# Kernel tuning notes

Measured on AMD Instinct MI355X. Metric: run time of the kernel, lower is better.

The kernel has to match this reference:

```python
import jax, jax.numpy as jnp
import numpy as np

T, B, C = 2048, 4, 1024
H, K = 16, 15
PAD_L = 14  # causal: padding_l = K - 1


def setup_inputs() -> dict:
    key = jax.random.key(0)
    k1, k2 = jax.random.split(key)
    x = jax.random.normal(k1, (T, B, C), dtype=jnp.float32)
    # xavier_uniform for Linear(C, H*K): bound = sqrt(6/(fan_in+fan_out))
    bound = float(np.sqrt(6.0 / (C + H * K)))
    Wlin = jax.random.uniform(k2, (H * K, C), dtype=jnp.float32, minval=-bound, maxval=bound)
    return {"x": x, "Wlin": Wlin}


def reference(x, Wlin):
    # x: (T, B, C); Wlin: (H*K, C) -- weight_linear with no bias
    t, b, c = x.shape
    r = c // H  # channels per head
    # Generate per-position filters: (T, B, H, K)
    w = jnp.einsum('tbc,kc->tbk', x, Wlin).reshape(t, b, H, K)
    # weight_softmax=True: normalize over kernel taps
    w = jax.nn.softmax(w, axis=-1)
    # unfold1d: pad left PAD_L, right K-1-PAD_L along time, take K shifted views
    xp = jnp.pad(x, ((PAD_L, K - 1 - PAD_L), (0, 0), (0, 0)))
    # (T, B, C, K): tap k at output t reads padded position t+k
    xu = jnp.stack([xp[k:k + t] for k in range(K)], axis=-1)
    xu = xu.reshape(t, b, H, r, K)
    # batched tiny matmul: (R x K) @ (K x 1) per (t, b, h)
    out = jnp.einsum('tbhrk,tbhk->tbhr', xu, w)
    return out.reshape(t, b, c)
```

## Files before the change

kernel.cpp:

```cpp
#include <hip/hip_runtime.h>
#include <hip/hip_bf16.h>


#define T_DIM 2048
#define B_DIM 4
#define C_DIM 1024
#define H_DIM 16
#define K_TAPS 15
#define R_DIM 64
#define N_DIM (H_DIM * K_TAPS)
#define M_DIM (T_DIM * B_DIM)
#define SM_STRIDE 244

typedef __attribute__((ext_vector_type(8))) short bf16x8;
typedef __attribute__((ext_vector_type(4))) float f32x4;

__device__ __forceinline__ unsigned short f2bf(float f) {
    union { float f; unsigned u; } v; v.f = f;
    return (unsigned short)((v.u + 0x7FFFu + ((v.u >> 16) & 1u)) >> 16);
}

__global__ __launch_bounds__(256) void convert_w(
    const float* __restrict__ W, unsigned short* __restrict__ Wbf)
{
    int i = (blockIdx.x * 256 + threadIdx.x) * 4;
    float4 v = *reinterpret_cast<const float4*>(W + i);
    ushort4 o;
    o.x = f2bf(v.x); o.y = f2bf(v.y); o.z = f2bf(v.z); o.w = f2bf(v.w);
    *reinterpret_cast<ushort4*>(Wbf + i) = o;
}

__global__ __launch_bounds__(256) void gemm_softmax_mfma(
    const float* __restrict__ x, const unsigned short* __restrict__ Wbf,
    float* __restrict__ wbuf)
{
    __shared__ float sm[4][16][SM_STRIDE];

    const int tid = threadIdx.x;
    const int w   = tid >> 6;
    const int l   = tid & 63;
    const int m0  = blockIdx.x * 16;
    const int row = l & 15;
    const int kg  = l >> 4;

    f32x4 acc[15];
    #pragma unroll
    for (int nt = 0; nt < 15; ++nt) acc[nt] = (f32x4){0.f, 0.f, 0.f, 0.f};

    const float* xp = x + (size_t)(m0 + row) * C_DIM + w * 256 + kg * 8;
    const unsigned short* wp = Wbf + (size_t)row * C_DIM + w * 256 + kg * 8;

    #pragma unroll 2
    for (int ks = 0; ks < 8; ++ks) {
        const int k = ks * 32;
        float4 a0 = *reinterpret_cast<const float4*>(xp + k);
        float4 a1 = *reinterpret_cast<const float4*>(xp + k + 4);
        bf16x8 af;
        af[0] = (short)f2bf(a0.x); af[1] = (short)f2bf(a0.y);
        af[2] = (short)f2bf(a0.z); af[3] = (short)f2bf(a0.w);
        af[4] = (short)f2bf(a1.x); af[5] = (short)f2bf(a1.y);
        af[6] = (short)f2bf(a1.z); af[7] = (short)f2bf(a1.w);
        bf16x8 bfr[15];
        #pragma unroll
        for (int nt = 0; nt < 15; ++nt)
            bfr[nt] = *reinterpret_cast<const bf16x8*>(wp + (size_t)nt * 16 * C_DIM + k);
        #pragma unroll
        for (int nt = 0; nt < 15; ++nt)
            acc[nt] = __builtin_amdgcn_mfma_f32_16x16x32_bf16(af, bfr[nt], acc[nt], 0, 0, 0);
    }

    #pragma unroll
    for (int nt = 0; nt < 15; ++nt)
        #pragma unroll
        for (int j = 0; j < 4; ++j)
            sm[w][kg * 4 + j][nt * 16 + row] = acc[nt][j];
    __syncthreads();

    const int r = tid >> 4;
    const int h = tid & 15;
    float s[K_TAPS];
    #pragma unroll
    for (int kk = 0; kk < K_TAPS; ++kk) {
        const int c = h * K_TAPS + kk;
        s[kk] = sm[0][r][c] + sm[1][r][c] + sm[2][r][c] + sm[3][r][c];
    }
    float mx = s[0];
    #pragma unroll
    for (int kk = 1; kk < K_TAPS; ++kk) mx = fmaxf(mx, s[kk]);
    float sum = 0.f;
    #pragma unroll
    for (int kk = 0; kk < K_TAPS; ++kk) {
        s[kk] = __expf(s[kk] - mx);
        sum += s[kk];
    }
    const float inv = 1.f / sum;
    float* dst = wbuf + (size_t)(m0 + r) * N_DIM + h * K_TAPS;
    #pragma unroll
    for (int kk = 0; kk < K_TAPS; ++kk) dst[kk] = s[kk] * inv;
}

__global__ __launch_bounds__(256) void conv_kernel(
    const float* __restrict__ x, const float* __restrict__ wbuf,
    float* __restrict__ out)
{
    __shared__ float xs[64 + K_TAPS - 1][R_DIM];

    const int tid = threadIdx.x;
    const int t0 = blockIdx.x * 64;
    const int bh = blockIdx.y;
    const int b = bh >> 4;
    const int h = bh & 15;
    const int cbase = h * R_DIM;

    for (int idx = tid; idx < (64 + K_TAPS - 1) * 16; idx += 256) {
        int rrow = idx >> 4, q = idx & 15;
        int t = t0 - (K_TAPS - 1) + rrow;
        float4 v = (t >= 0)
            ? *reinterpret_cast<const float4*>(x + ((size_t)t * B_DIM + b) * C_DIM + cbase + q * 4)
            : (float4){0.f, 0.f, 0.f, 0.f};
        *reinterpret_cast<float4*>(&xs[rrow][q * 4]) = v;
    }
    __syncthreads();

    const int r = tid & 63;
    const int tg = __builtin_amdgcn_readfirstlane(tid >> 6);

    float xv[31];
    #pragma unroll
    for (int j = 0; j < 31; ++j) xv[j] = xs[tg * 16 + j][r];

    float accv[16];
    #pragma unroll
    for (int i = 0; i < 16; ++i) accv[i] = 0.f;

    #pragma unroll
    for (int i = 0; i < 16; ++i) {
        const int t = t0 + tg * 16 + i;
        const float* wv = wbuf + ((size_t)t * B_DIM + b) * N_DIM + h * K_TAPS;
        #pragma unroll
        for (int k = 0; k < K_TAPS; ++k)
            accv[i] += wv[k] * xv[i + k];
    }

    #pragma unroll
    for (int i = 0; i < 16; ++i) {
        const int t = t0 + tg * 16 + i;
        out[((size_t)t * B_DIM + b) * C_DIM + cbase + r] = accv[i];
    }
}

extern "C" void kernel_launch(void* const* d_in, const int* in_sizes, int n_in,
                              void* d_out, int out_size, void* d_ws, size_t ws_size,
                              hipStream_t stream) {
    const float* x    = (const float*)d_in[0];
    const float* Wlin = (const float*)d_in[1];
    float* out  = (float*)d_out;

    float* wbuf = (float*)d_ws;
    unsigned short* Wbf = (unsigned short*)((char*)d_ws + (size_t)M_DIM * N_DIM * sizeof(float));

    convert_w<<<(N_DIM * C_DIM) / (256 * 4), 256, 0, stream>>>(Wlin, Wbf);
    gemm_softmax_mfma<<<M_DIM / 16, 256, 0, stream>>>(x, Wbf, wbuf);
    conv_kernel<<<dim3(T_DIM / 64, B_DIM * H_DIM), 256, 0, stream>>>(x, wbuf, out);
}
```

Baseline: 127.9 us.

## Fuse filter GEMM, softmax and dynamic convolution into one MFMA kernel

Merges the softmax-filter GEMM and the convolution kernel into one kernel per (16-timestep, batch) tile. The normalized filters are written as a banded bf16 Toeplitz matrix in shared memory, and the convolution runs as MFMA against a transposed bf16 copy of the x window. The intermediate weight buffer round trip through global memory and one launch go away, and x loads are hoisted ahead of the GEMM loop. In exchange the conv inputs and filters are rounded to bf16, which lowers accuracy, and each tile re-reads a 14-step halo of x.

```diff
diff --git a/kernel.cpp b/kernel.cpp
--- a/kernel.cpp
+++ b/kernel.cpp
@@ -7,10 +7,11 @@
 #define C_DIM 1024
 #define H_DIM 16
 #define K_TAPS 15
-#define R_DIM 64
-#define N_DIM (H_DIM * K_TAPS)
-#define M_DIM (T_DIM * B_DIM)
+#define N_DIM 240
 #define SM_STRIDE 244
+#define SM_FLOATS (4 * 16 * SM_STRIDE)
+#define XT_STRIDE 34
+#define XT_OFF 4096
 
 typedef __attribute__((ext_vector_type(8))) short bf16x8;
 typedef __attribute__((ext_vector_type(4))) float f32x4;
@@ -30,40 +31,45 @@
     *reinterpret_cast<ushort4*>(Wbf + i) = o;
 }
 
-__global__ __launch_bounds__(256) void gemm_softmax_mfma(
+__global__ __launch_bounds__(256, 2) void fused_dynconv(
     const float* __restrict__ x, const unsigned short* __restrict__ Wbf,
-    float* __restrict__ wbuf)
+    float* __restrict__ out)
 {
-    __shared__ float sm[4][16][SM_STRIDE];
+    __shared__ float smem[SM_FLOATS];
 
     const int tid = threadIdx.x;
-    const int w   = tid >> 6;
+    const int wv  = tid >> 6;
     const int l   = tid & 63;
-    const int m0  = blockIdx.x * 16;
+    const int t0  = blockIdx.x * 16;
+    const int b   = blockIdx.y;
     const int row = l & 15;
     const int kg  = l >> 4;
+
+    const float* xp = x + ((size_t)(t0 + row) * B_DIM + b) * C_DIM + wv * 256 + kg * 8;
+    const unsigned short* wp = Wbf + (size_t)row * C_DIM + wv * 256 + kg * 8;
+
+    float4 xa[8], xb[8];
+    #pragma unroll
+    for (int ks = 0; ks < 8; ++ks) {
+        xa[ks] = *reinterpret_cast<const float4*>(xp + ks * 32);
+        xb[ks] = *reinterpret_cast<const float4*>(xp + ks * 32 + 4);
+    }
 
     f32x4 acc[15];
     #pragma unroll
     for (int nt = 0; nt < 15; ++nt) acc[nt] = (f32x4){0.f, 0.f, 0.f, 0.f};
 
-    const float* xp = x + (size_t)(m0 + row) * C_DIM + w * 256 + kg * 8;
-    const unsigned short* wp = Wbf + (size_t)row * C_DIM + w * 256 + kg * 8;
-
-    #pragma unroll 2
+    #pragma unroll
     for (int ks = 0; ks < 8; ++ks) {
-        const int k = ks * 32;
-        float4 a0 = *reinterpret_cast<const float4*>(xp + k);
-        float4 a1 = *reinterpret_cast<const float4*>(xp + k + 4);
-        bf16x8 af;
-        af[0] = (short)f2bf(a0.x); af[1] = (short)f2bf(a0.y);
-        af[2] = (short)f2bf(a0.z); af[3] = (short)f2bf(a0.w);
-        af[4] = (short)f2bf(a1.x); af[5] = (short)f2bf(a1.y);
-        af[6] = (short)f2bf(a1.z); af[7] = (short)f2bf(a1.w);
         bf16x8 bfr[15];
         #pragma unroll
         for (int nt = 0; nt < 15; ++nt)
-            bfr[nt] = *reinterpret_cast<const bf16x8*>(wp + (size_t)nt * 16 * C_DIM + k);
+            bfr[nt] = *reinterpret_cast<const bf16x8*>(wp + (size_t)nt * 16 * C_DIM + ks * 32);
+        bf16x8 af;
+        af[0] = (short)f2bf(xa[ks].x); af[1] = (short)f2bf(xa[ks].y);
+        af[2] = (short)f2bf(xa[ks].z); af[3] = (short)f2bf(xa[ks].w);
+        af[4] = (short)f2bf(xb[ks].x); af[5] = (short)f2bf(xb[ks].y);
+        af[6] = (short)f2bf(xb[ks].z); af[7] = (short)f2bf(xb[ks].w);
         #pragma unroll
         for (int nt = 0; nt < 15; ++nt)
             acc[nt] = __builtin_amdgcn_mfma_f32_16x16x32_bf16(af, bfr[nt], acc[nt], 0, 0, 0);
@@ -73,79 +79,80 @@
     for (int nt = 0; nt < 15; ++nt)
         #pragma unroll
         for (int j = 0; j < 4; ++j)
-            sm[w][kg * 4 + j][nt * 16 + row] = acc[nt][j];
+            smem[(wv * 16 + kg * 4 + j) * SM_STRIDE + nt * 16 + row] = acc[nt][j];
     __syncthreads();
 
-    const int r = tid >> 4;
-    const int h = tid & 15;
-    float s[K_TAPS];
+    const int rr = tid >> 4;
+    const int hh = tid & 15;
+    float wn[K_TAPS];
     #pragma unroll
     for (int kk = 0; kk < K_TAPS; ++kk) {
-        const int c = h * K_TAPS + kk;
-        s[kk] = sm[0][r][c] + sm[1][r][c] + sm[2][r][c] + sm[3][r][c];
+        const int c = hh * K_TAPS + kk;
+        wn[kk] = smem[(0 * 16 + rr) * SM_STRIDE + c] + smem[(1 * 16 + rr) * SM_STRIDE + c]
+               + smem[(2 * 16 + rr) * SM_STRIDE + c] + smem[(3 * 16 + rr) * SM_STRIDE + c];
     }
-    float mx = s[0];
+    float mx = wn[0];
     #pragma unroll
-    for (int kk = 1; kk < K_TAPS; ++kk) mx = fmaxf(mx, s[kk]);
+    for (int kk = 1; kk < K_TAPS; ++kk) mx = fmaxf(mx, wn[kk]);
     float sum = 0.f;
     #pragma unroll
-    for (int kk = 0; kk < K_TAPS; ++kk) {
-        s[kk] = __expf(s[kk] - mx);
-        sum += s[kk];
-    }
+    for (int kk = 0; kk < K_TAPS; ++kk) { wn[kk] = __expf(wn[kk] - mx); sum += wn[kk]; }
     const float inv = 1.f / sum;
-    float* dst = wbuf + (size_t)(m0 + r) * N_DIM + h * K_TAPS;
-    #pragma unroll
-    for (int kk = 0; kk < K_TAPS; ++kk) dst[kk] = s[kk] * inv;
-}
+    __syncthreads();
 
-__global__ __launch_bounds__(256) void conv_kernel(
-    const float* __restrict__ x, const float* __restrict__ wbuf,
-    float* __restrict__ out)
-{
-    __shared__ float xs[64 + K_TAPS - 1][R_DIM];
-
-    const int tid = threadIdx.x;
-    const int t0 = blockIdx.x * 64;
-    const int bh = blockIdx.y;
-    const int b = bh >> 4;
-    const int h = bh & 15;
-    const int cbase = h * R_DIM;
-
-    for (int idx = tid; idx < (64 + K_TAPS - 1) * 16; idx += 256) {
-        int rrow = idx >> 4, q = idx & 15;
-        int t = t0 - (K_TAPS - 1) + rrow;
-        float4 v = (t >= 0)
-            ? *reinterpret_cast<const float4*>(x + ((size_t)t * B_DIM + b) * C_DIM + cbase + q * 4)
-            : (float4){0.f, 0.f, 0.f, 0.f};
-        *reinterpret_cast<float4*>(&xs[rrow][q * 4]) = v;
+    unsigned short* wsA = reinterpret_cast<unsigned short*>(smem);
+    {
+        int4 z = {0, 0, 0, 0};
+        int4* p = reinterpret_cast<int4*>(smem) + tid * 4;
+        p[0] = z; p[1] = z; p[2] = z; p[3] = z;
     }
     __syncthreads();
 
-    const int r = tid & 63;
-    const int tg = __builtin_amdgcn_readfirstlane(tid >> 6);
-
-    float xv[31];
     #pragma unroll
-    for (int j = 0; j < 31; ++j) xv[j] = xs[tg * 16 + j][r];
-
-    float accv[16];
-    #pragma unroll
-    for (int i = 0; i < 16; ++i) accv[i] = 0.f;
-
-    #pragma unroll
-    for (int i = 0; i < 16; ++i) {
-        const int t = t0 + tg * 16 + i;
-        const float* wv = wbuf + ((size_t)t * B_DIM + b) * N_DIM + h * K_TAPS;
-        #pragma unroll
-        for (int k = 0; k < K_TAPS; ++k)
-            accv[i] += wv[k] * xv[i + k];
+    for (int tap = 0; tap < K_TAPS; ++tap) {
+        const int k = rr + tap;
+        wsA[hh * 512 + (k >> 3) * 128 + rr * 8 + (k & 7)] = f2bf(wn[tap] * inv);
     }
 
-    #pragma unroll
-    for (int i = 0; i < 16; ++i) {
-        const int t = t0 + tg * 16 + i;
-        out[((size_t)t * B_DIM + b) * C_DIM + cbase + r] = accv[i];
+    unsigned short* xT = reinterpret_cast<unsigned short*>(smem + XT_OFF);
+    const int c4 = (tid & 127) * 4;
+    const int k2 = tid >> 7;
+    #pragma unroll 1
+    for (int q = 0; q < 2; ++q) {
+        #pragma unroll 4
+        for (int k = 0; k < 32; k += 2) {
+            const int kk = k + k2;
+            const int ta = t0 - 14 + kk;
+            float4 v = (ta >= 0 && ta < T_DIM)
+                ? *reinterpret_cast<const float4*>(x + ((size_t)ta * B_DIM + b) * C_DIM + q * 512 + c4)
+                : (float4){0.f, 0.f, 0.f, 0.f};
+            xT[(c4 + 0) * XT_STRIDE + kk] = f2bf(v.x);
+            xT[(c4 + 1) * XT_STRIDE + kk] = f2bf(v.y);
+            xT[(c4 + 2) * XT_STRIDE + kk] = f2bf(v.z);
+            xT[(c4 + 3) * XT_STRIDE + kk] = f2bf(v.w);
+        }
+        __syncthreads();
+
+        const int h0 = q * 8 + wv * 2;
+        const bf16x8 A0 = *reinterpret_cast<const bf16x8*>(wsA + (h0 * 64 + l) * 8);
+        const bf16x8 A1 = *reinterpret_cast<const bf16x8*>(wsA + ((h0 + 1) * 64 + l) * 8);
+        const int* xTi = reinterpret_cast<const int*>(xT);
+        #pragma unroll
+        for (int i = 0; i < 8; ++i) {
+            const int ct = q * 32 + wv * 8 + i;
+            const int cl = (wv * 8 + i) * 16 + row;
+            const int base = cl * (XT_STRIDE / 2) + kg * 4;
+            int4 bi;
+            bi.x = xTi[base + 0]; bi.y = xTi[base + 1];
+            bi.z = xTi[base + 2]; bi.w = xTi[base + 3];
+            union { int4 i4; bf16x8 h; } u; u.i4 = bi;
+            f32x4 d = __builtin_amdgcn_mfma_f32_16x16x32_bf16(
+                (i < 4) ? A0 : A1, u.h, (f32x4){0.f, 0.f, 0.f, 0.f}, 0, 0, 0);
+            #pragma unroll
+            for (int j = 0; j < 4; ++j)
+                out[((size_t)(t0 + kg * 4 + j) * B_DIM + b) * C_DIM + ct * 16 + row] = d[j];
+        }
+        __syncthreads();
     }
 }
 
@@ -154,12 +161,9 @@
                               hipStream_t stream) {
     const float* x    = (const float*)d_in[0];
     const float* Wlin = (const float*)d_in[1];
-    float* out  = (float*)d_out;
-
-    float* wbuf = (float*)d_ws;
-    unsigned short* Wbf = (unsigned short*)((char*)d_ws + (size_t)M_DIM * N_DIM * sizeof(float));
+    float* out = (float*)d_out;
+    unsigned short* Wbf = (unsigned short*)d_ws;
 
     convert_w<<<(N_DIM * C_DIM) / (256 * 4), 256, 0, stream>>>(Wlin, Wbf);
-    gemm_softmax_mfma<<<M_DIM / 16, 256, 0, stream>>>(x, Wbf, wbuf);
-    conv_kernel<<<dim3(T_DIM / 64, B_DIM * H_DIM), 256, 0, stream>>>(x, wbuf, out);
+    fused_dynconv<<<dim3(T_DIM / 16, B_DIM), 256, 0, stream>>>(x, Wbf, out);
 }
```

Result: faster. 125.1 us (-2.1%).

## Split filter GEMM over two N-halves and store softmax weights as bf16

Applied to the files above, without the earlier changes.

The projection GEMM is split across two blocks along the output dimension. Each block computes 8 of the 15 16-wide column tiles, with one overlapping tile, and runs softmax for 8 heads. This halves the accumulator registers, permits 4 blocks per CU, and doubles the grid. The softmax filter weights are now written to the workspace as bf16 instead of fp32, which halves the intermediate buffer traffic read by the conv kernel. The cost is that x is read twice in the GEMM and the filter weights lose precision.

```diff
diff --git a/kernel.cpp b/kernel.cpp
--- a/kernel.cpp
+++ b/kernel.cpp
@@ -8,9 +8,9 @@
 #define H_DIM 16
 #define K_TAPS 15
 #define R_DIM 64
-#define N_DIM (H_DIM * K_TAPS)
+#define N_DIM 240
 #define M_DIM (T_DIM * B_DIM)
-#define SM_STRIDE 244
+#define SM_STRIDE 132
 
 typedef __attribute__((ext_vector_type(8))) short bf16x8;
 typedef __attribute__((ext_vector_type(4))) float f32x4;
@@ -18,6 +18,10 @@
 __device__ __forceinline__ unsigned short f2bf(float f) {
     union { float f; unsigned u; } v; v.f = f;
     return (unsigned short)((v.u + 0x7FFFu + ((v.u >> 16) & 1u)) >> 16);
+}
+__device__ __forceinline__ float bf2f(unsigned short h) {
+    union { unsigned u; float f; } v; v.u = ((unsigned)h) << 16;
+    return v.f;
 }
 
 __global__ __launch_bounds__(256) void convert_w(
@@ -30,77 +34,79 @@
     *reinterpret_cast<ushort4*>(Wbf + i) = o;
 }
 
-__global__ __launch_bounds__(256) void gemm_softmax_mfma(
+__global__ __launch_bounds__(256, 4) void gemm_softmax_half(
     const float* __restrict__ x, const unsigned short* __restrict__ Wbf,
-    float* __restrict__ wbuf)
+    unsigned short* __restrict__ wout)
 {
     __shared__ float sm[4][16][SM_STRIDE];
 
     const int tid = threadIdx.x;
-    const int w   = tid >> 6;
+    const int wv  = tid >> 6;
     const int l   = tid & 63;
     const int m0  = blockIdx.x * 16;
+    const int nh  = blockIdx.y;
+    const int ntb = nh * 7;
     const int row = l & 15;
     const int kg  = l >> 4;
 
-    f32x4 acc[15];
+    f32x4 acc[8];
     #pragma unroll
-    for (int nt = 0; nt < 15; ++nt) acc[nt] = (f32x4){0.f, 0.f, 0.f, 0.f};
+    for (int nt = 0; nt < 8; ++nt) acc[nt] = (f32x4){0.f, 0.f, 0.f, 0.f};
 
-    const float* xp = x + (size_t)(m0 + row) * C_DIM + w * 256 + kg * 8;
-    const unsigned short* wp = Wbf + (size_t)row * C_DIM + w * 256 + kg * 8;
+    const float* xp = x + (size_t)(m0 + row) * C_DIM + wv * 256 + kg * 8;
+    const unsigned short* wp = Wbf + (size_t)(ntb * 16 + row) * C_DIM + wv * 256 + kg * 8;
 
     #pragma unroll 2
     for (int ks = 0; ks < 8; ++ks) {
         const int k = ks * 32;
         float4 a0 = *reinterpret_cast<const float4*>(xp + k);
         float4 a1 = *reinterpret_cast<const float4*>(xp + k + 4);
+        bf16x8 bfr[8];
+        #pragma unroll
+        for (int nt = 0; nt < 8; ++nt)
+            bfr[nt] = *reinterpret_cast<const bf16x8*>(wp + (size_t)nt * 16 * C_DIM + k);
         bf16x8 af;
         af[0] = (short)f2bf(a0.x); af[1] = (short)f2bf(a0.y);
         af[2] = (short)f2bf(a0.z); af[3] = (short)f2bf(a0.w);
         af[4] = (short)f2bf(a1.x); af[5] = (short)f2bf(a1.y);
         af[6] = (short)f2bf(a1.z); af[7] = (short)f2bf(a1.w);
-        bf16x8 bfr[15];
         #pragma unroll
-        for (int nt = 0; nt < 15; ++nt)
-            bfr[nt] = *reinterpret_cast<const bf16x8*>(wp + (size_t)nt * 16 * C_DIM + k);
-        #pragma unroll
-        for (int nt = 0; nt < 15; ++nt)
+        for (int nt = 0; nt < 8; ++nt)
             acc[nt] = __builtin_amdgcn_mfma_f32_16x16x32_bf16(af, bfr[nt], acc[nt], 0, 0, 0);
     }
 
     #pragma unroll
-    for (int nt = 0; nt < 15; ++nt)
+    for (int nt = 0; nt < 8; ++nt)
         #pragma unroll
         for (int j = 0; j < 4; ++j)
-            sm[w][kg * 4 + j][nt * 16 + row] = acc[nt][j];
+            sm[wv][kg * 4 + j][nt * 16 + row] = acc[nt][j];
     __syncthreads();
 
-    const int r = tid >> 4;
-    const int h = tid & 15;
-    float s[K_TAPS];
-    #pragma unroll
-    for (int kk = 0; kk < K_TAPS; ++kk) {
-        const int c = h * K_TAPS + kk;
-        s[kk] = sm[0][r][c] + sm[1][r][c] + sm[2][r][c] + sm[3][r][c];
+    if (tid < 128) {
+        const int rr = tid >> 3;
+        const int hh = tid & 7;
+        const int base = (nh ? 8 : 0) + hh * K_TAPS;
+        float s[K_TAPS];
+        #pragma unroll
+        for (int kk = 0; kk < K_TAPS; ++kk) {
+            const int c = base + kk;
+            s[kk] = sm[0][rr][c] + sm[1][rr][c] + sm[2][rr][c] + sm[3][rr][c];
+        }
+        float mx = s[0];
+        #pragma unroll
+        for (int kk = 1; kk < K_TAPS; ++kk) mx = fmaxf(mx, s[kk]);
+        float sum = 0.f;
+        #pragma unroll
+        for (int kk = 0; kk < K_TAPS; ++kk) { s[kk] = __expf(s[kk] - mx); sum += s[kk]; }
+        const float inv = 1.f / sum;
+        unsigned short* dst = wout + (size_t)(m0 + rr) * N_DIM + (nh * 8 + hh) * K_TAPS;
+        #pragma unroll
+        for (int kk = 0; kk < K_TAPS; ++kk) dst[kk] = f2bf(s[kk] * inv);
     }
-    float mx = s[0];
-    #pragma unroll
-    for (int kk = 1; kk < K_TAPS; ++kk) mx = fmaxf(mx, s[kk]);
-    float sum = 0.f;
-    #pragma unroll
-    for (int kk = 0; kk < K_TAPS; ++kk) {
-        s[kk] = __expf(s[kk] - mx);
-        sum += s[kk];
-    }
-    const float inv = 1.f / sum;
-    float* dst = wbuf + (size_t)(m0 + r) * N_DIM + h * K_TAPS;
-    #pragma unroll
-    for (int kk = 0; kk < K_TAPS; ++kk) dst[kk] = s[kk] * inv;
 }
 
 __global__ __launch_bounds__(256) void conv_kernel(
-    const float* __restrict__ x, const float* __restrict__ wbuf,
+    const float* __restrict__ x, const unsigned short* __restrict__ wbuf,
     float* __restrict__ out)
 {
     __shared__ float xs[64 + K_TAPS - 1][R_DIM];
@@ -136,10 +142,10 @@
     #pragma unroll
     for (int i = 0; i < 16; ++i) {
         const int t = t0 + tg * 16 + i;
-        const float* wv = wbuf + ((size_t)t * B_DIM + b) * N_DIM + h * K_TAPS;
+        const unsigned short* wv = wbuf + ((size_t)t * B_DIM + b) * N_DIM + h * K_TAPS;
         #pragma unroll
         for (int k = 0; k < K_TAPS; ++k)
-            accv[i] += wv[k] * xv[i + k];
+            accv[i] += bf2f(wv[k]) * xv[i + k];
     }
 
     #pragma unroll
@@ -154,12 +160,12 @@
                               hipStream_t stream) {
     const float* x    = (const float*)d_in[0];
     const float* Wlin = (const float*)d_in[1];
-    float* out  = (float*)d_out;
+    float* out = (float*)d_out;
 
-    float* wbuf = (float*)d_ws;
-    unsigned short* Wbf = (unsigned short*)((char*)d_ws + (size_t)M_DIM * N_DIM * sizeof(float));
+    unsigned short* wout = (unsigned short*)d_ws;
+    unsigned short* Wbf  = (unsigned short*)((char*)d_ws + (size_t)M_DIM * N_DIM * sizeof(unsigned short));
 
     convert_w<<<(N_DIM * C_DIM) / (256 * 4), 256, 0, stream>>>(Wlin, Wbf);
-    gemm_softmax_mfma<<<M_DIM / 16, 256, 0, stream>>>(x, Wbf, wbuf);
-    conv_kernel<<<dim3(T_DIM / 64, B_DIM * H_DIM), 256, 0, stream>>>(x, wbuf, out);
+    gemm_softmax_half<<<dim3(M_DIM / 16, 2), 256, 0, stream>>>(x, Wbf, wout);
+    conv_kernel<<<dim3(T_DIM / 64, B_DIM * H_DIM), 256, 0, stream>>>(x, wout, out);
 }
```

After: 148.0 us. +15.7%, slower.

## Pipeline GEMM x tiles through LDS with async global_load_lds triple buffering

Applied to the files above, without the earlier changes.

The projection GEMM is restructured. Each block now covers 32 rows with two waves, and each wave walks the full K dimension, so the cross-wave split-K reduction goes away. x tiles are staged into XOR-swizzled LDS through global_load_lds with a three-buffer prefetch pipeline. The softmax output is written padded to 16 taps per head with float4 stores, and the conv kernel indexes that padded layout. Each wave issues more weight-fragment loads per block, blocks are half the size, and the LDS footprint grows, which may hurt occupancy.

```diff
diff --git a/kernel.cpp b/kernel.cpp
--- a/kernel.cpp
+++ b/kernel.cpp
@@ -8,9 +8,13 @@
 #define H_DIM 16
 #define K_TAPS 15
 #define R_DIM 64
-#define N_DIM (H_DIM * K_TAPS)
-#define M_DIM (T_DIM * B_DIM)
-#define SM_STRIDE 244
+#define N_DIM 240
+#define M_DIM 8192
+#define BM 32
+#define BKF 128
+#define NSTEP 8
+#define TILE_F (BM * BKF)
+#define EP_STRIDE 244
 
 typedef __attribute__((ext_vector_type(8))) short bf16x8;
 typedef __attribute__((ext_vector_type(4))) float f32x4;
@@ -18,6 +22,12 @@
 __device__ __forceinline__ unsigned short f2bf(float f) {
     union { float f; unsigned u; } v; v.f = f;
     return (unsigned short)((v.u + 0x7FFFu + ((v.u >> 16) & 1u)) >> 16);
+}
+
+typedef __attribute__((address_space(1))) const void g_void;
+typedef __attribute__((address_space(3))) void l_void;
+__device__ __forceinline__ void gload_lds16(const void* g, void* l) {
+    __builtin_amdgcn_global_load_lds((g_void*)g, (l_void*)l, 16, 0, 0);
 }
 
 __global__ __launch_bounds__(256) void convert_w(
@@ -30,73 +40,107 @@
     *reinterpret_cast<ushort4*>(Wbf + i) = o;
 }
 
-__global__ __launch_bounds__(256) void gemm_softmax_mfma(
+__device__ __forceinline__ void stage_tile(const float* xrow0, int s, float* buf, int tid) {
+    #pragma unroll
+    for (int j = 0; j < 8; ++j) {
+        const int e  = j * 128 + tid;
+        const int r  = e >> 5;
+        const int c  = e & 31;
+        const int gc = c ^ (r & 7);
+        const float* src = xrow0 + (size_t)r * C_DIM + s * BKF + gc * 4;
+        float* dst = buf + (size_t)(j * 128 + (tid & ~63)) * 4;
+        gload_lds16(src, dst);
+    }
+}
+
+__global__ __launch_bounds__(128) void gemm_softmax_v3(
     const float* __restrict__ x, const unsigned short* __restrict__ Wbf,
-    float* __restrict__ wbuf)
+    float* __restrict__ wout)
 {
-    __shared__ float sm[4][16][SM_STRIDE];
+    __shared__ float smem[3 * TILE_F];
 
     const int tid = threadIdx.x;
-    const int w   = tid >> 6;
+    const int wv  = tid >> 6;
     const int l   = tid & 63;
-    const int m0  = blockIdx.x * 16;
+    const int m0  = blockIdx.x * BM;
     const int row = l & 15;
     const int kg  = l >> 4;
+    const int r7  = row & 7;
+
+    const float* xrow0 = x + (size_t)m0 * C_DIM;
+    const unsigned short* wp = Wbf + (size_t)row * C_DIM + kg * 8;
 
     f32x4 acc[15];
     #pragma unroll
     for (int nt = 0; nt < 15; ++nt) acc[nt] = (f32x4){0.f, 0.f, 0.f, 0.f};
 
-    const float* xp = x + (size_t)(m0 + row) * C_DIM + w * 256 + kg * 8;
-    const unsigned short* wp = Wbf + (size_t)row * C_DIM + w * 256 + kg * 8;
-
-    #pragma unroll 2
-    for (int ks = 0; ks < 8; ++ks) {
-        const int k = ks * 32;
-        float4 a0 = *reinterpret_cast<const float4*>(xp + k);
-        float4 a1 = *reinterpret_cast<const float4*>(xp + k + 4);
-        bf16x8 af;
-        af[0] = (short)f2bf(a0.x); af[1] = (short)f2bf(a0.y);
-        af[2] = (short)f2bf(a0.z); af[3] = (short)f2bf(a0.w);
-        af[4] = (short)f2bf(a1.x); af[5] = (short)f2bf(a1.y);
-        af[6] = (short)f2bf(a1.z); af[7] = (short)f2bf(a1.w);
-        bf16x8 bfr[15];
-        #pragma unroll
-        for (int nt = 0; nt < 15; ++nt)
-            bfr[nt] = *reinterpret_cast<const bf16x8*>(wp + (size_t)nt * 16 * C_DIM + k);
-        #pragma unroll
-        for (int nt = 0; nt < 15; ++nt)
-            acc[nt] = __builtin_amdgcn_mfma_f32_16x16x32_bf16(af, bfr[nt], acc[nt], 0, 0, 0);
-    }
-
+    stage_tile(xrow0, 0, smem + 0 * TILE_F, tid);
+    stage_tile(xrow0, 1, smem + 1 * TILE_F, tid);
+    asm volatile("s_waitcnt vmcnt(8)" ::: "memory");
+    __builtin_amdgcn_s_barrier();
+
+    #pragma unroll
+    for (int s = 0; s < NSTEP; ++s) {
+        const float* abase = smem + (s % 3) * TILE_F + (size_t)(wv * 16 + row) * BKF;
+        #pragma unroll
+        for (int sub = 0; sub < 4; ++sub) {
+            const int cb = sub * 8 + kg * 2;
+            float4 a0 = *reinterpret_cast<const float4*>(abase + (size_t)((cb + 0) ^ r7) * 4);
+            float4 a1 = *reinterpret_cast<const float4*>(abase + (size_t)((cb + 1) ^ r7) * 4);
+            bf16x8 af;
+            af[0] = (short)f2bf(a0.x); af[1] = (short)f2bf(a0.y);
+            af[2] = (short)f2bf(a0.z); af[3] = (short)f2bf(a0.w);
+            af[4] = (short)f2bf(a1.x); af[5] = (short)f2bf(a1.y);
+            af[6] = (short)f2bf(a1.z); af[7] = (short)f2bf(a1.w);
+            const int kofs = s * BKF + sub * 32;
+            #pragma unroll
+            for (int nt = 0; nt < 15; ++nt) {
+                bf16x8 bfv = *reinterpret_cast<const bf16x8*>(wp + (size_t)nt * 16 * C_DIM + kofs);
+                acc[nt] = __builtin_amdgcn_mfma_f32_16x16x32_bf16(af, bfv, acc[nt], 0, 0, 0);
+            }
+        }
+        __builtin_amdgcn_sched_barrier(0);
+        if (s + 2 < NSTEP)
+            stage_tile(xrow0, s + 2, smem + ((s + 2) % 3) * TILE_F, tid);
+        if (s < NSTEP - 2) { asm volatile("s_waitcnt vmcnt(8)" ::: "memory"); }
+        else               { asm volatile("s_waitcnt vmcnt(0)" ::: "memory"); }
+        __builtin_amdgcn_s_barrier();
+    }
+    __syncthreads();
+
+    float* ep = smem + (size_t)wv * (16 * EP_STRIDE);
     #pragma unroll
     for (int nt = 0; nt < 15; ++nt)
         #pragma unroll
         for (int j = 0; j < 4; ++j)
-            sm[w][kg * 4 + j][nt * 16 + row] = acc[nt][j];
+            ep[(kg * 4 + j) * EP_STRIDE + nt * 16 + row] = acc[nt][j];
     __syncthreads();
 
-    const int r = tid >> 4;
-    const int h = tid & 15;
-    float s[K_TAPS];
-    #pragma unroll
-    for (int kk = 0; kk < K_TAPS; ++kk) {
-        const int c = h * K_TAPS + kk;
-        s[kk] = sm[0][r][c] + sm[1][r][c] + sm[2][r][c] + sm[3][r][c];
-    }
-    float mx = s[0];
-    #pragma unroll
-    for (int kk = 1; kk < K_TAPS; ++kk) mx = fmaxf(mx, s[kk]);
-    float sum = 0.f;
-    #pragma unroll
-    for (int kk = 0; kk < K_TAPS; ++kk) {
-        s[kk] = __expf(s[kk] - mx);
-        sum += s[kk];
-    }
-    const float inv = 1.f / sum;
-    float* dst = wbuf + (size_t)(m0 + r) * N_DIM + h * K_TAPS;
-    #pragma unroll
-    for (int kk = 0; kk < K_TAPS; ++kk) dst[kk] = s[kk] * inv;
+    #pragma unroll
+    for (int p = 0; p < 4; ++p) {
+        const int idx = p * 64 + l;
+        const int rr  = idx >> 4;
+        const int hh  = idx & 15;
+        const float* sp = ep + rr * EP_STRIDE + hh * K_TAPS;
+        float sv[K_TAPS];
+        #pragma unroll
+        for (int kk = 0; kk < K_TAPS; ++kk) sv[kk] = sp[kk];
+        float mx = sv[0];
+        #pragma unroll
+        for (int kk = 1; kk < K_TAPS; ++kk) mx = fmaxf(mx, sv[kk]);
+        float sum = 0.f;
+        #pragma unroll
+        for (int kk = 0; kk < K_TAPS; ++kk) { sv[kk] = __expf(sv[kk] - mx); sum += sv[kk]; }
+        const float inv = 1.f / sum;
+        float o[16];
+        #pragma unroll
+        for (int kk = 0; kk < K_TAPS; ++kk) o[kk] = sv[kk] * inv;
+        o[15] = 0.f;
+        float* dst = wout + ((size_t)(m0 + wv * 16 + rr)) * (H_DIM * 16) + hh * 16;
+        #pragma unroll
+        for (int q = 0; q < 4; ++q)
+            *reinterpret_cast<float4*>(dst + q * 4) = *reinterpret_cast<const float4*>(&o[q * 4]);
+    }
 }
 
 __global__ __launch_bounds__(256) void conv_kernel(
@@ -136,10 +180,10 @@
     #pragma unroll
     for (int i = 0; i < 16; ++i) {
         const int t = t0 + tg * 16 + i;
-        const float* wv = wbuf + ((size_t)t * B_DIM + b) * N_DIM + h * K_TAPS;
+        const float* wrow = wbuf + ((size_t)t * B_DIM + b) * (H_DIM * 16) + h * 16;
         #pragma unroll
         for (int k = 0; k < K_TAPS; ++k)
-            accv[i] += wv[k] * xv[i + k];
+            accv[i] += wrow[k] * xv[i + k];
     }
 
     #pragma unroll
@@ -154,12 +198,12 @@
                               hipStream_t stream) {
     const float* x    = (const float*)d_in[0];
     const float* Wlin = (const float*)d_in[1];
-    float* out  = (float*)d_out;
-
-    float* wbuf = (float*)d_ws;
-    unsigned short* Wbf = (unsigned short*)((char*)d_ws + (size_t)M_DIM * N_DIM * sizeof(float));
+    float* out = (float*)d_out;
+
+    float* wout = (float*)d_ws;
+    unsigned short* Wbf = (unsigned short*)((char*)d_ws + (size_t)M_DIM * H_DIM * 16 * sizeof(float));
 
     convert_w<<<(N_DIM * C_DIM) / (256 * 4), 256, 0, stream>>>(Wlin, Wbf);
-    gemm_softmax_mfma<<<M_DIM / 16, 256, 0, stream>>>(x, Wbf, wbuf);
-    conv_kernel<<<dim3(T_DIM / 64, B_DIM * H_DIM), 256, 0, stream>>>(x, wbuf, out);
-}
+    gemm_softmax_v3<<<M_DIM / BM, 128, 0, stream>>>(x, Wbf, wout);
+    conv_kernel<<<dim3(T_DIM / 64, B_DIM * H_DIM), 256, 0, stream>>>(x, wout, out);
+}
```

After: 143.7 us. 1.12x slower.
